# Kernel tuning notes

Measured on AMD Instinct MI355X. Metric: run time of the kernel, lower is better.

## Reference

```python
import jax, jax.numpy as jnp
import numpy as np

N, B, E, H, D, L, NT = 30000, 16, 60000, 128, 64, 2, 5


def _build_graph():
    rng = np.random.default_rng(0)
    ng = N // B
    row = rng.integers(0, N, size=E)
    g = row // ng
    col = g * ng + rng.integers(0, ng, size=E)  # bonds stay within a graph
    order = np.argsort(g, kind='stable')        # sort bonds by graph id
    row, col = row[order], col[order]
    edge_index = np.stack([row, col]).astype(np.int32)
    # bond graph: bonds adjacent iff they share an atom (vectorized _build_bond_graph)
    atoms = np.concatenate([row, col])
    bonds = np.concatenate([np.arange(E), np.arange(E)])
    o2 = np.argsort(atoms, kind='stable')
    sb = bonds[o2]
    counts = np.bincount(atoms, minlength=N)
    offs = np.concatenate([[0], np.cumsum(counts)[:-1]])
    sq = counts * counts
    total = int(sq.sum())
    gid = np.repeat(np.arange(N), sq)
    poff = np.concatenate([[0], np.cumsum(sq)[:-1]])
    pos = np.arange(total) - np.repeat(poff, sq)
    c, o = counts[gid], offs[gid]
    ii, jj = pos // c, pos % c
    mask = ii != jj
    bond_edge_index = np.stack([sb[o + ii][mask], sb[o + jj][mask]]).astype(np.int32)
    batch = np.repeat(np.arange(B), ng).astype(np.int32)
    return edge_index, bond_edge_index, batch


def setup_inputs() -> dict:
    edge_index, bond_edge_index, batch = _build_graph()
    key = jax.random.key(0)
    ks = jax.random.split(key, 16)
    s = 0.05
    n = lambda k, shp: jax.random.normal(k, shp, jnp.float32) * s
    return {
        'atom_features': jax.random.normal(ks[0], (N, H), jnp.float32),
        'atom_pos': jax.random.normal(ks[1], (N, 3), jnp.float32),
        'atomic_numbers': jax.random.randint(ks[2], (N,), 1, 20, jnp.int32),
        'batch': jnp.asarray(batch),
        'edge_index': jnp.asarray(edge_index),
        'bond_edge_index': jnp.asarray(bond_edge_index),
        'iw1': n(ks[3], (2 * H, D)), 'ib1': jnp.zeros((D,), jnp.float32),
        'iw2': n(ks[4], (D, D)), 'ib2': jnp.zeros((D,), jnp.float32),
        'emb': n(ks[5], (L, NT, D)),
        'mw1': n(ks[6], (L, 3 * D, D)), 'mb1': jnp.zeros((L, D), jnp.float32),
        'mw2': n(ks[7], (L, D, D)), 'mb2': jnp.zeros((L, D), jnp.float32),
        'uw1': n(ks[8], (L, 2 * D, D)), 'ub1': jnp.zeros((L, D), jnp.float32),
        'uw2': n(ks[9], (L, D, D)), 'ub2': jnp.zeros((L, D), jnp.float32),
        'num_graphs': B,
    }


def reference(atom_features, atom_pos, iw1, ib1, iw2, ib2, emb, mw1, mb1, mw2, mb2,
              uw1, ub1, uw2, ub2, atomic_numbers, batch, edge_index, bond_edge_index,
              num_graphs):
    row, col = edge_index
    hi, hj = atom_features[row], atom_features[col]  # [E, H] gathers
    # bond_init MLP
    x = jax.nn.silu(jnp.concatenate([hi, hj], -1) @ iw1 + ib1) @ iw2 + ib2  # [E, D]
    # _classify_bonds: cosine-similarity thresholds (order matters, matches torch)
    ni = jnp.maximum(jnp.linalg.norm(hi, axis=-1), 1e-8)
    nj = jnp.maximum(jnp.linalg.norm(hj, axis=-1), 1e-8)
    sim = jnp.sum(hi * hj, -1) / (ni * nj)
    bt = jnp.where(sim > 0.8, 1, 0)
    bt = jnp.where(sim > 0.9, 2, bt)
    bt = jnp.where(sim < 0.3, 3, bt)
    src, dst = bond_edge_index  # x_j = x[src], x_i = x[dst]; aggregate at dst
    nb = x.shape[0]
    deg = jax.ops.segment_sum(jnp.ones(src.shape, jnp.float32), dst, num_segments=nb)
    denom = jnp.maximum(deg, 1.0)[:, None]  # PyG mean aggr: 0 for isolated nodes
    for l in range(mw1.shape[0]):
        te = emb[l][bt]  # [E, D] bond-type embedding
        msg_in = jnp.concatenate([x[dst], x[src], te[dst]], -1)  # [BE, 3D]
        msg = jax.nn.silu(msg_in @ mw1[l] + mb1[l]) @ mw2[l] + mb2[l]
        aggr = jax.ops.segment_sum(msg, dst, num_segments=nb) / denom
        upd_in = jnp.concatenate([aggr, x], -1)
        x = x + jax.nn.silu(upd_in @ uw1[l] + ub1[l]) @ uw2[l] + ub2[l]
    # pooling: edges are sorted by graph, so repeat_interleave == batch[row]
    bond_batch = batch[row]
    cnt = jax.ops.segment_sum(jnp.ones((nb,), jnp.float32), bond_batch, num_segments=num_graphs)
    gfeat = jax.ops.segment_sum(x, bond_batch, num_segments=num_graphs) / jnp.maximum(cnt, 1.0)[:, None]
    return x, gfeat
```

## Files before the change

kernel.cpp:

```cpp
#include <hip/hip_runtime.h>
#include <cstdint>
#include <cstddef>

#define HDIM 128
#define DDIM 64
#define NTYPES 5
#define NGRAPHS 16
#define PCHUNK 128
#define EPB 64
#define APW 8

typedef __attribute__((ext_vector_type(8))) short short8;
typedef __attribute__((ext_vector_type(4))) float f32x4;

static __device__ __forceinline__ short8 as_s8(uint4 u) {
    return __builtin_bit_cast(short8, u);
}

static __device__ __forceinline__ float silu_f(float v) {
    return v * __builtin_amdgcn_rcpf(1.0f + __expf(-v));
}

static __device__ __forceinline__ float4 ld4(const float* p) {
    return *reinterpret_cast<const float4*>(p);
}

static __device__ __forceinline__ void st4(float* p, float4 v) {
    *reinterpret_cast<float4*>(p) = v;
}

static __device__ __forceinline__ float4 add4(float4 a, float4 b) {
    return make_float4(a.x + b.x, a.y + b.y, a.z + b.z, a.w + b.w);
}

static __device__ __forceinline__ void silu_acc4(float4& s, float4 v) {
    s.x += silu_f(v.x);
    s.y += silu_f(v.y);
    s.z += silu_f(v.z);
    s.w += silu_f(v.w);
}

static __device__ __forceinline__ unsigned int bf16r(float f) {
    unsigned int u = __float_as_uint(f);
    return (u + 0x7FFFu + ((u >> 16) & 1u)) >> 16;
}
static __device__ __forceinline__ unsigned int cvtpk(float a, float b) {
    unsigned int r;
    asm("v_cvt_pk_bf16_f32 %0, %1, %2" : "=v"(r) : "v"(a), "v"(b));
    return r;
}
static __device__ __forceinline__ uint4 pack8(const float* f) {
    uint4 r;
    r.x = cvtpk(f[0], f[1]);
    r.y = cvtpk(f[2], f[3]);
    r.z = cvtpk(f[4], f[5]);
    r.w = cvtpk(f[6], f[7]);
    return r;
}
static __device__ __forceinline__ void unpack8(uint4 u, float4& a, float4& b) {
    a.x = __uint_as_float(u.x << 16);
    a.y = __uint_as_float(u.x & 0xFFFF0000u);
    a.z = __uint_as_float(u.y << 16);
    a.w = __uint_as_float(u.y & 0xFFFF0000u);
    b.x = __uint_as_float(u.z << 16);
    b.y = __uint_as_float(u.z & 0xFFFF0000u);
    b.z = __uint_as_float(u.w << 16);
    b.w = __uint_as_float(u.w & 0xFFFF0000u);
}

static __device__ __forceinline__ void hilo8(const float* f, uint4& h, uint4& lo) {
    h = pack8(f);
    float4 a, b;
    unpack8(h, a, b);
    lo.x = cvtpk(f[0] - a.x, f[1] - a.y);
    lo.y = cvtpk(f[2] - a.z, f[3] - a.w);
    lo.z = cvtpk(f[4] - b.x, f[5] - b.y);
    lo.w = cvtpk(f[6] - b.z, f[7] - b.w);
}

static __device__ __forceinline__ int xcd_logical_block() {
    int chunk = (int)(gridDim.x >> 3);
    return (int)(blockIdx.x & 7) * chunk + (int)(blockIdx.x >> 3);
}

__global__ void __launch_bounds__(256) count_k(const int* __restrict__ bdst,
                                               int* __restrict__ cnt, int BE) {
    int i = blockIdx.x * 256 + threadIdx.x;
    if (i < BE)
        __hip_atomic_fetch_add(&cnt[bdst[i]], 1, __ATOMIC_RELAXED, __HIP_MEMORY_SCOPE_AGENT);
}

__global__ void __launch_bounds__(256) bsum_k(const int* __restrict__ cnt,
                                              int* __restrict__ bsum, int E) {
    __shared__ int red[256];
    int t = threadIdx.x;
    int i = blockIdx.x * 256 + t;
    red[t] = (i < E) ? cnt[i] : 0;
    __syncthreads();
    #pragma unroll
    for (int off = 128; off > 0; off >>= 1) {
        if (t < off) red[t] += red[t + off];
        __syncthreads();
    }
    if (t == 0) bsum[blockIdx.x] = red[0];
}

__global__ void __launch_bounds__(1024) bscan_k(const int* __restrict__ bsum,
                                                int* __restrict__ bpre, int NB) {
    __shared__ int sh[1024];
    int t = threadIdx.x;
    int v0 = (t < NB) ? bsum[t] : 0;
    sh[t] = v0;
    __syncthreads();
    for (int off = 1; off < 1024; off <<= 1) {
        int v = (t >= off) ? sh[t - off] : 0;
        __syncthreads();
        sh[t] += v;
        __syncthreads();
    }
    if (t < NB) bpre[t] = sh[t] - v0;
}

__global__ void __launch_bounds__(256) offs_k(const int* __restrict__ cnt,
                                              const int* __restrict__ bpre,
                                              int* __restrict__ offs,
                                              int* __restrict__ cursor, int E) {
    __shared__ int sh[256];
    int t = threadIdx.x;
    int i = blockIdx.x * 256 + t;
    int v0 = (i < E) ? cnt[i] : 0;
    sh[t] = v0;
    __syncthreads();
    for (int off = 1; off < 256; off <<= 1) {
        int v = (t >= off) ? sh[t - off] : 0;
        __syncthreads();
        sh[t] += v;
        __syncthreads();
    }
    int ex = sh[t] - v0 + bpre[blockIdx.x];
    if (i < E) { offs[i] = ex; cursor[i] = ex; }
    if (i == E - 1) offs[E] = ex + v0;
}

__global__ void __launch_bounds__(256) scatter_k(const int* __restrict__ bsrc,
                                                 const int* __restrict__ bdst,
                                                 int* __restrict__ cursor,
                                                 int* __restrict__ srclist, int BE) {
    int i = blockIdx.x * 256 + threadIdx.x;
    if (i < BE) {
        int d = bdst[i];
        int p = __hip_atomic_fetch_add(&cursor[d], 1, __ATOMIC_RELAXED,
                                       __HIP_MEMORY_SCOPE_AGENT);
        srclist[p] = bsrc[i];
    }
}

__global__ void __launch_bounds__(64) prep_k(const float* __restrict__ emb,
                                             const float* __restrict__ mw1,
                                             const float* __restrict__ mb1,
                                             const float* __restrict__ mw2,
                                             const float* __restrict__ mb2,
                                             const float* __restrict__ uw1,
                                             const float* __restrict__ uw2,
                                             const float* __restrict__ iw2,
                                             float* __restrict__ tt,
                                             float* __restrict__ b2u,
                                             uint4* __restrict__ fw2u,
                                             uint4* __restrict__ fu1b,
                                             uint4* __restrict__ fu2,
                                             uint4* __restrict__ fp,
                                             uint4* __restrict__ fiw2,
                                             uint4* __restrict__ fp0) {
    int b = blockIdx.x;
    int l = threadIdx.x;
    if (b < 10) {
        int ll = b / NTYPES, t = b % NTYPES;
        const float* embl = emb + (size_t)ll * NTYPES * DDIM + (size_t)t * DDIM;
        const float* w1 = mw1 + (size_t)ll * 192 * DDIM;
        float s = mb1[ll * DDIM + l];
        #pragma unroll 8
        for (int k = 0; k < DDIM; ++k)
            s = fmaf(embl[k], w1[(HDIM + k) * DDIM + l], s);
        tt[(size_t)b * DDIM + l] = s;
        return;
    }
    if (b < 12) {
        int ll = b - 10;
        const float* u1 = uw1 + (size_t)ll * 128 * DDIM;
        float s = 0.f;
        #pragma unroll 8
        for (int t = 0; t < DDIM; ++t)
            s = fmaf(mb2[ll * DDIM + t], u1[(size_t)t * DDIM + l], s);
        b2u[ll * DDIM + l] = s;
        return;
    }
    int pb = b - 12;
    int mat = pb >> 3, jt = (pb >> 1) & 3, ks = pb & 1;
    int k0 = ks * 32 + (l >> 4) * 8;
    int j = jt * 16 + (l & 15);
    float f[8];
    uint4* dst;
    if (mat <= 1) {
        const float* w2 = mw2 + (size_t)mat * DDIM * DDIM;
        const float* u1 = uw1 + (size_t)mat * 128 * DDIM;
        #pragma unroll
        for (int i = 0; i < 8; ++i) {
            float s = 0.f;
            #pragma unroll 8
            for (int t = 0; t < DDIM; ++t)
                s = fmaf(w2[(size_t)(k0 + i) * DDIM + t], u1[(size_t)t * DDIM + j], s);
            f[i] = s;
        }
        dst = fw2u + (size_t)mat * 1024;
    } else {
        const float* src;
        switch (mat) {
            case 2:  src = uw1 + 64 * 64;                   dst = fu1b;        break;
            case 3:  src = uw1 + 128 * 64 + 64 * 64;        dst = fu1b + 1024; break;
            case 4:  src = uw2;                             dst = fu2;         break;
            case 5:  src = uw2 + 4096;                      dst = fu2 + 1024;  break;
            case 6:  src = mw1 + (size_t)192 * 64;          dst = fp;          break;
            case 7:  src = mw1 + (size_t)192 * 64 + 64 * 64; dst = fp + 1024;  break;
            case 8:  src = iw2;                             dst = fiw2;        break;
            case 9:  src = mw1;                             dst = fp0;         break;
            default: src = mw1 + (size_t)64 * 64;           dst = fp0 + 1024;  break;
        }
        #pragma unroll
        for (int i = 0; i < 8; ++i) f[i] = src[(size_t)(k0 + i) * DDIM + j];
    }
    uint4 h, lo;
    hilo8(f, h, lo);
    size_t di = ((size_t)(jt * 2 + ks) * 64 + l) * 2;
    dst[di] = h;
    dst[di + 1] = lo;
}

static __device__ __forceinline__ int slotIdx(int row, int slot) {
    return row * 8 + (slot ^ (row & 7));
}

static __device__ __forceinline__ short8 ldFragA(const uint4* buf, int rowBase, int lane, int ks) {
    int row = rowBase + (lane & 15);
    int slot = ks * 4 + (lane >> 4);
    return as_s8(buf[slotIdx(row, slot)]);
}

static __device__ __forceinline__ void loadB(const uint4* __restrict__ frag, int jt, int lane,
                                             short8& h0, short8& h1, short8& l0, short8& l1) {
    const uint4* p0 = frag + ((size_t)(jt * 2 + 0) * 64 + lane) * 2;
    const uint4* p1 = frag + ((size_t)(jt * 2 + 1) * 64 + lane) * 2;
    h0 = as_s8(p0[0]); l0 = as_s8(p0[1]);
    h1 = as_s8(p1[0]); l1 = as_s8(p1[1]);
}

static __device__ __forceinline__ f32x4 gemm_tile(const uint4* Ahi, const uint4* Alo,
        int rowBase, int lane,
        short8 bh0, short8 bh1, short8 bl0, short8 bl1, f32x4 acc) {
    short8 ah0 = ldFragA(Ahi, rowBase, lane, 0);
    short8 ah1 = ldFragA(Ahi, rowBase, lane, 1);
    short8 al0 = ldFragA(Alo, rowBase, lane, 0);
    short8 al1 = ldFragA(Alo, rowBase, lane, 1);
    acc = __builtin_amdgcn_mfma_f32_16x16x32_bf16(ah0, bh0, acc, 0, 0, 0);
    acc = __builtin_amdgcn_mfma_f32_16x16x32_bf16(ah1, bh1, acc, 0, 0, 0);
    acc = __builtin_amdgcn_mfma_f32_16x16x32_bf16(al0, bh0, acc, 0, 0, 0);
    acc = __builtin_amdgcn_mfma_f32_16x16x32_bf16(al1, bh1, acc, 0, 0, 0);
    acc = __builtin_amdgcn_mfma_f32_16x16x32_bf16(ah0, bl0, acc, 0, 0, 0);
    acc = __builtin_amdgcn_mfma_f32_16x16x32_bf16(ah1, bl1, acc, 0, 0, 0);
    return acc;
}

__global__ void __launch_bounds__(256) atom_proj_k(
    const float* __restrict__ AF, const float* __restrict__ iw1,
    float* __restrict__ pa, float* __restrict__ qa, float* __restrict__ na, int N) {
    int lane = threadIdx.x & 63;
    int w = __builtin_amdgcn_readfirstlane((int)(threadIdx.x >> 6));
    int abase = blockIdx.x * (4 * APW) + w * APW;
    if (abase >= N) return;

    float accp[APW], accq[APW], nrm[APW];
    #pragma unroll
    for (int a = 0; a < APW; ++a) { accp[a] = 0.f; accq[a] = 0.f; nrm[a] = 0.f; }

    #pragma unroll 4
    for (int k = 0; k < HDIM; k += 4) {
        float wt[4], wb[4];
        #pragma unroll
        for (int kk = 0; kk < 4; ++kk) {
            wt[kk] = iw1[(size_t)(k + kk) * DDIM + lane];
            wb[kk] = iw1[(size_t)(HDIM + k + kk) * DDIM + lane];
        }
        #pragma unroll
        for (int a = 0; a < APW; ++a) {
            int aa = min(abase + a, N - 1);
            float4 hv = ld4(AF + (size_t)aa * HDIM + k);
            accp[a] = fmaf(hv.x, wt[0], accp[a]);
            accp[a] = fmaf(hv.y, wt[1], accp[a]);
            accp[a] = fmaf(hv.z, wt[2], accp[a]);
            accp[a] = fmaf(hv.w, wt[3], accp[a]);
            accq[a] = fmaf(hv.x, wb[0], accq[a]);
            accq[a] = fmaf(hv.y, wb[1], accq[a]);
            accq[a] = fmaf(hv.z, wb[2], accq[a]);
            accq[a] = fmaf(hv.w, wb[3], accq[a]);
            nrm[a] = fmaf(hv.x, hv.x, nrm[a]);
            nrm[a] = fmaf(hv.y, hv.y, nrm[a]);
            nrm[a] = fmaf(hv.z, hv.z, nrm[a]);
            nrm[a] = fmaf(hv.w, hv.w, nrm[a]);
        }
    }
    #pragma unroll
    for (int a = 0; a < APW; ++a) {
        int atom = abase + a;
        if (atom < N) {
            pa[(size_t)atom * DDIM + lane] = accp[a];
            qa[(size_t)atom * DDIM + lane] = accq[a];
            if (lane == 0) na[atom] = sqrtf(nrm[a]);
        }
    }
}

__global__ void __launch_bounds__(512, 4) bond_init2_k(
    const float* __restrict__ AF, const int* __restrict__ row, const int* __restrict__ col,
    const float* __restrict__ pa, const float* __restrict__ qa, const float* __restrict__ na,
    const float* __restrict__ b1, const uint4* __restrict__ fW2, const float* __restrict__ b2,
    const uint4* __restrict__ fP0,
    float* __restrict__ x, int* __restrict__ bt,
    float* __restrict__ pd, uint4* __restrict__ ps, int E) {
    __shared__ uint4 sAhi[512];
    __shared__ uint4 sAlo[512];
    __shared__ uint4 sXhi[512];
    __shared__ uint4 sXlo[512];
    int nEB = (E + EPB - 1) / EPB;
    int lb = xcd_logical_block();
    if (lb >= nEB) return;
    int tid = threadIdx.x;
    int lane = tid & 63;
    int w = __builtin_amdgcn_readfirstlane((int)(tid >> 6));
    int e0 = lb * EPB;

    {
        int dl = tid >> 3, q = tid & 7;
        int d = e0 + dl;
        bool ok = d < E;
        int dd = ok ? d : 0;
        int r = row[dd], c = col[dd];
        int jq = q * 8;

        const float* hi = AF + (size_t)r * HDIM + q * 16;
        const float* hj = AF + (size_t)c * HDIM + q * 16;
        float dt = 0.f;
        #pragma unroll
        for (int k = 0; k < 16; k += 4) {
            float4 a4 = ld4(hi + k), b4 = ld4(hj + k);
            dt += a4.x * b4.x + a4.y * b4.y + a4.z * b4.z + a4.w * b4.w;
        }
        dt += __shfl_xor(dt, 1, 64);
        dt += __shfl_xor(dt, 2, 64);
        dt += __shfl_xor(dt, 4, 64);
        if (q == 0 && ok) {
            float nr = fmaxf(na[r], 1e-8f), nc = fmaxf(na[c], 1e-8f);
            float sim = dt / (nr * nc);
            int t = 0;
            if (sim > 0.8f) t = 1;
            if (sim > 0.9f) t = 2;
            if (sim < 0.3f) t = 3;
            bt[d] = t;
        }

        const float* pr = pa + (size_t)r * DDIM + jq;
        const float* qc = qa + (size_t)c * DDIM + jq;
        float4 p0 = ld4(pr + 0), p1 = ld4(pr + 4);
        float4 q0 = ld4(qc + 0), q1 = ld4(qc + 4);
        float hv[8];
        hv[0] = silu_f(p0.x + q0.x + b1[jq + 0]);
        hv[1] = silu_f(p0.y + q0.y + b1[jq + 1]);
        hv[2] = silu_f(p0.z + q0.z + b1[jq + 2]);
        hv[3] = silu_f(p0.w + q0.w + b1[jq + 3]);
        hv[4] = silu_f(p1.x + q1.x + b1[jq + 4]);
        hv[5] = silu_f(p1.y + q1.y + b1[jq + 5]);
        hv[6] = silu_f(p1.z + q1.z + b1[jq + 6]);
        hv[7] = silu_f(p1.w + q1.w + b1[jq + 7]);
        if (!ok) {
            #pragma unroll
            for (int i = 0; i < 8; ++i) hv[i] = 0.f;
        }
        uint4 h4, l4;
        hilo8(hv, h4, l4);
        int si = slotIdx(dl, q);
        sAhi[si] = h4; sAlo[si] = l4;
    }
    int jt = w & 3, mh = w >> 2;
    short8 W2h0, W2h1, W2l0, W2l1;
    loadB(fW2, jt, lane, W2h0, W2h1, W2l0, W2l1);
    __syncthreads();

    int rb0 = mh * 32, rb1 = mh * 32 + 16;
    f32x4 z4 = {0.f, 0.f, 0.f, 0.f};
    f32x4 acc0 = gemm_tile(sAhi, sAlo, rb0, lane, W2h0, W2h1, W2l0, W2l1, z4);
    f32x4 acc1 = gemm_tile(sAhi, sAlo, rb1, lane, W2h0, W2h1, W2l0, W2l1, z4);
// ... 40 lines not shown
        int jd = jp * 16 + (lane & 15);
        #pragma unroll
        for (int mt = 0; mt < 4; ++mt) {
            f32x4 qq = (mt == 0) ? q0 : (mt == 1) ? q1 : (mt == 2) ? q2 : q3;
            #pragma unroll
            for (int r = 0; r < 4; ++r) {
                int rowi = mt * 16 + (lane >> 4) * 4 + r;
                int e = e0 + rowi;
                if (e < E) pd[(size_t)e * DDIM + jd] = qq[r];
            }
        }
    } else {
        int js = jp * 16 + (lane & 15);
        #pragma unroll
        for (int mt = 0; mt < 4; ++mt) {
            f32x4 qq = (mt == 0) ? q0 : (mt == 1) ? q1 : (mt == 2) ? q2 : q3;
            #pragma unroll
            for (int r = 0; r < 4; ++r) {
                int rowi = mt * 16 + (lane >> 4) * 4 + r;
                int ui = (rowi * 8 + ((js >> 3) ^ (rowi & 7))) * 8 + (js & 7);
                hA[ui] = (unsigned short)bf16r(qq[r]);
            }
        }
    }
    __syncthreads();
    {
        int dl = tid >> 3, q = tid & 7;
        int d = e0 + dl;
        if (d < E) ps[(size_t)d * 8 + q] = sAhi[slotIdx(dl, q)];
    }
}

__global__ void __launch_bounds__(256) proj_k(const float* __restrict__ x,
                                              const float* __restrict__ w1 ,
                                              float* __restrict__ pd, uint4* __restrict__ ps,
                                              int E) {
    int lane = threadIdx.x & 63;
    int w = __builtin_amdgcn_readfirstlane((int)(threadIdx.x >> 6));
    int e = blockIdx.x * EPB + lane;
    bool ok = e < E;
    int eidx = ok ? e : 0;
    int j0 = w * 16;
    const float* xr = x + (size_t)eidx * DDIM;

    float apd[16], aps[16];
    #pragma unroll
    for (int jj = 0; jj < 16; ++jj) { apd[jj] = 0.f; aps[jj] = 0.f; }
    #pragma unroll 2
    for (int c = 0; c < 16; ++c) {
        float4 v = ld4(xr + c * 4);
        float xv[4] = {v.x, v.y, v.z, v.w};
        #pragma unroll
        for (int kk = 0; kk < 4; ++kk) {
            int k = c * 4 + kk;
            const float* wd = w1 + (size_t)k * DDIM + j0;
            const float* wsv = w1 + (size_t)(DDIM + k) * DDIM + j0;
            #pragma unroll
            for (int jj = 0; jj < 16; ++jj) {
                apd[jj] = fmaf(xv[kk], wd[jj], apd[jj]);
                aps[jj] = fmaf(xv[kk], wsv[jj], aps[jj]);
            }
        }
    }
    if (ok) {
        float* pr = pd + (size_t)e * DDIM + j0;
        st4(pr + 0,  make_float4(apd[0],  apd[1],  apd[2],  apd[3]));
        st4(pr + 4,  make_float4(apd[4],  apd[5],  apd[6],  apd[7]));
        st4(pr + 8,  make_float4(apd[8],  apd[9],  apd[10], apd[11]));
        st4(pr + 12, make_float4(apd[12], apd[13], apd[14], apd[15]));
        ps[(size_t)e * 8 + 2 * w + 0] = pack8(aps + 0);
        ps[(size_t)e * 8 + 2 * w + 1] = pack8(aps + 8);
    }
}

__global__ void __launch_bounds__(512, 4) layer_k(
    float* __restrict__ x, const float* __restrict__ pd, const uint4* __restrict__ ps,
    const float* __restrict__ tt_l, const int* __restrict__ bt,
    const int* __restrict__ offs, const int* __restrict__ srclist,
    const int* __restrict__ cnt,
    const uint4* __restrict__ fW2u, const float* __restrict__ b2u,
    const uint4* __restrict__ fU1b, const float* __restrict__ ub1,
    const uint4* __restrict__ fU2, const float* __restrict__ ub2,
    const uint4* __restrict__ fP ,
    float* __restrict__ pdn, uint4* __restrict__ psn, int E) {
    __shared__ uint4 sAhi[512];
    __shared__ uint4 sAlo[512];
    __shared__ uint4 sXhi[512];
    __shared__ uint4 sXlo[512];
    __shared__ float degLDS[64];
    int nEB = (E + EPB - 1) / EPB;
    int lb = xcd_logical_block();
    if (lb >= nEB) return;
    int tid = threadIdx.x;
    int lane = tid & 63;
    int w = __builtin_amdgcn_readfirstlane((int)(tid >> 6));
    int e0 = lb * EPB;

    {
        int dl = tid >> 3, q = tid & 7;
        int d = e0 + dl;
        bool ok = d < E;
        int dd = ok ? d : 0;
        int jq = q * 8;
        const float* xr = x + (size_t)dd * DDIM + jq;
        float4 xv0 = ld4(xr + 0), xv1 = ld4(xr + 4);
        int dc = cnt[dd];
        const float* pr = pd + (size_t)dd * DDIM + jq;
        const float* tp = tt_l + (size_t)bt[dd] * DDIM + jq;
        float4 b0 = add4(ld4(pr + 0), ld4(tp + 0));
        float4 b1 = add4(ld4(pr + 4), ld4(tp + 4));
        float4 s0 = make_float4(0, 0, 0, 0), s1 = s0;
        int p0 = ok ? offs[d] : 0, p1 = ok ? offs[d + 1] : 0;
        int p = p0;
        for (; p + 4 <= p1; p += 4) {
            uint4 u0 = ps[(size_t)srclist[p + 0] * 8 + q];
            uint4 u1 = ps[(size_t)srclist[p + 1] * 8 + q];
            uint4 u2 = ps[(size_t)srclist[p + 2] * 8 + q];
            uint4 u3 = ps[(size_t)srclist[p + 3] * 8 + q];
            float4 a, b;
            unpack8(u0, a, b);
            silu_acc4(s0, add4(b0, a));
            silu_acc4(s1, add4(b1, b));
            unpack8(u1, a, b);
            silu_acc4(s0, add4(b0, a));
            silu_acc4(s1, add4(b1, b));
            unpack8(u2, a, b);
            silu_acc4(s0, add4(b0, a));
            silu_acc4(s1, add4(b1, b));
            unpack8(u3, a, b);
            silu_acc4(s0, add4(b0, a));
            silu_acc4(s1, add4(b1, b));
        }
        for (; p < p1; ++p) {
            uint4 u0 = ps[(size_t)srclist[p] * 8 + q];
            float4 a, b;
            unpack8(u0, a, b);
            silu_acc4(s0, add4(b0, a));
            silu_acc4(s1, add4(b1, b));
        }
        float inv = 1.0f / fmaxf((float)dc, 1.0f);
        float sv[8] = {s0.x * inv, s0.y * inv, s0.z * inv, s0.w * inv,
                       s1.x * inv, s1.y * inv, s1.z * inv, s1.w * inv};
        float xf[8] = {xv0.x, xv0.y, xv0.z, xv0.w, xv1.x, xv1.y, xv1.z, xv1.w};
        if (!ok) {
            #pragma unroll
            for (int i = 0; i < 8; ++i) { sv[i] = 0.f; xf[i] = 0.f; }
        }
        uint4 h4, l4;
        int si = slotIdx(dl, q);
        hilo8(sv, h4, l4);
        sAhi[si] = h4; sAlo[si] = l4;
        hilo8(xf, h4, l4);
        sXhi[si] = h4; sXlo[si] = l4;
        if (q == 0) degLDS[dl] = (ok && dc > 0) ? 1.0f : 0.0f;
    }
    int jt = w & 3, mh = w >> 2;
    short8 A2h0, A2h1, A2l0, A2l1;
    short8 U1h0, U1h1, U1l0, U1l1;
    loadB(fW2u, jt, lane, A2h0, A2h1, A2l0, A2l1);
    loadB(fU1b, jt, lane, U1h0, U1h1, U1l0, U1l1);
    __syncthreads();

    int rb0 = mh * 32, rb1 = mh * 32 + 16;
    f32x4 z4 = {0.f, 0.f, 0.f, 0.f};
    f32x4 acc0 = z4, acc1 = z4;
    acc0 = gemm_tile(sAhi, sAlo, rb0, lane, A2h0, A2h1, A2l0, A2l1, acc0);
    acc0 = gemm_tile(sXhi, sXlo, rb0, lane, U1h0, U1h1, U1l0, U1l1, acc0);
    acc1 = gemm_tile(sAhi, sAlo, rb1, lane, A2h0, A2h1, A2l0, A2l1, acc1);
    acc1 = gemm_tile(sXhi, sXlo, rb1, lane, U1h0, U1h1, U1l0, U1l1, acc1);
    __syncthreads();
    int j = jt * 16 + (lane & 15);
    float ub1j = ub1[j], b2uj = b2u[j];
    unsigned short* hA = (unsigned short*)sAhi;
    unsigned short* lA = (unsigned short*)sAlo;
    #pragma unroll
    for (int r = 0; r < 4; ++r) {
        int row = rb0 + (lane >> 4) * 4 + r;
        float hv = silu_f(acc0[r] + ub1j + degLDS[row] * b2uj);
        unsigned int hb = bf16r(hv);
        float lov = hv - __uint_as_float(hb << 16);
        int ui = (row * 8 + ((j >> 3) ^ (row & 7))) * 8 + (j & 7);
        hA[ui] = (unsigned short)hb;
        lA[ui] = (unsigned short)bf16r(lov);
    }
    #pragma unroll
    for (int r = 0; r < 4; ++r) {
        int row = rb1 + (lane >> 4) * 4 + r;
        float hv = silu_f(acc1[r] + ub1j + degLDS[row] * b2uj);
        unsigned int hb = bf16r(hv);
        float lov = hv - __uint_as_float(hb << 16);
        int ui = (row * 8 + ((j >> 3) ^ (row & 7))) * 8 + (j & 7);
        hA[ui] = (unsigned short)hb;
        lA[ui] = (unsigned short)bf16r(lov);
    }
    __syncthreads();

    short8 U2h0, U2h1, U2l0, U2l1;
    loadB(fU2, jt, lane, U2h0, U2h1, U2l0, U2l1);
    f32x4 o0 = gemm_tile(sAhi, sAlo, rb0, lane, U2h0, U2h1, U2l0, U2l1, z4);
    f32x4 o1 = gemm_tile(sAhi, sAlo, rb1, lane, U2h0, U2h1, U2l0, U2l1, z4);
    float ub2j = ub2[j];
    bool haveP = (fP != nullptr);
    unsigned short* hX = (unsigned short*)sXhi;
    unsigned short* lX = (unsigned short*)sXlo;
    #pragma unroll
    for (int r = 0; r < 4; ++r) {
        int row = rb0 + (lane >> 4) * 4 + r;
        int e = e0 + row;
        int ui = (row * 8 + ((j >> 3) ^ (row & 7))) * 8 + (j & 7);
        float xvv = __uint_as_float((unsigned int)hX[ui] << 16)
                  + __uint_as_float((unsigned int)lX[ui] << 16);
        float xn = xvv + o0[r] + ub2j;
        if (e < E) x[(size_t)e * DDIM + j] = xn;
        if (haveP) {
            unsigned int hb = bf16r(xn);
            float lov = xn - __uint_as_float(hb << 16);
            hX[ui] = (unsigned short)hb;
            lX[ui] = (unsigned short)bf16r(lov);
        }
    }
    #pragma unroll
    for (int r = 0; r < 4; ++r) {
        int row = rb1 + (lane >> 4) * 4 + r;
        int e = e0 + row;
        int ui = (row * 8 + ((j >> 3) ^ (row & 7))) * 8 + (j & 7);
        float xvv = __uint_as_float((unsigned int)hX[ui] << 16)
                  + __uint_as_float((unsigned int)lX[ui] << 16);
        float xn = xvv + o1[r] + ub2j;
        if (e < E) x[(size_t)e * DDIM + j] = xn;
        if (haveP) {
            unsigned int hb = bf16r(xn);
            float lov = xn - __uint_as_float(hb << 16);
            hX[ui] = (unsigned short)hb;
            lX[ui] = (unsigned short)bf16r(lov);
        }
    }
    if (!haveP) return;
    __syncthreads();

    const uint4* fPw = (w < 4) ? fP : (fP + 1024);
    int jp = w & 3;
    short8 Ph0, Ph1, Pl0, Pl1;
    loadB(fPw, jp, lane, Ph0, Ph1, Pl0, Pl1);
    f32x4 q0 = gemm_tile(sXhi, sXlo, 0,  lane, Ph0, Ph1, Pl0, Pl1, z4);
    f32x4 q1 = gemm_tile(sXhi, sXlo, 16, lane, Ph0, Ph1, Pl0, Pl1, z4);
    f32x4 q2 = gemm_tile(sXhi, sXlo, 32, lane, Ph0, Ph1, Pl0, Pl1, z4);
    f32x4 q3 = gemm_tile(sXhi, sXlo, 48, lane, Ph0, Ph1, Pl0, Pl1, z4);
    if (w < 4) {
        int jd = jp * 16 + (lane & 15);
        #pragma unroll
        for (int mt = 0; mt < 4; ++mt) {
            f32x4 qq = (mt == 0) ? q0 : (mt == 1) ? q1 : (mt == 2) ? q2 : q3;
            #pragma unroll
            for (int r = 0; r < 4; ++r) {
                int row = mt * 16 + (lane >> 4) * 4 + r;
                int e = e0 + row;
                if (e < E) pdn[(size_t)e * DDIM + jd] = qq[r];
            }
        }
    } else {
        int js = jp * 16 + (lane & 15);
        #pragma unroll
        for (int mt = 0; mt < 4; ++mt) {
            f32x4 qq = (mt == 0) ? q0 : (mt == 1) ? q1 : (mt == 2) ? q2 : q3;
            #pragma unroll
            for (int r = 0; r < 4; ++r) {
                int row = mt * 16 + (lane >> 4) * 4 + r;
                int ui = (row * 8 + ((js >> 3) ^ (row & 7))) * 8 + (js & 7);
                hA[ui] = (unsigned short)bf16r(qq[r]);
            }
        }
    }
    __syncthreads();
    {
        int dl = tid >> 3, q = tid & 7;
        int d = e0 + dl;
        if (d < E) psn[(size_t)d * 8 + q] = sAhi[slotIdx(dl, q)];
    }
}

__global__ void __launch_bounds__(256) pool_k(
    const float* __restrict__ x, const int* __restrict__ row,
    const int* __restrict__ batch, float* __restrict__ gfeat, int E) {
    int lane = threadIdx.x & 63;
    int esub = threadIdx.x >> 6;
    int e0 = blockIdx.x * PCHUNK;
    int e1 = min(e0 + PCHUNK, E);
    float sum = 0.f;
    int cur = -1;
    for (int e = e0 + esub; e < e1; e += 4) {
        int g = batch[row[e]];
        if (g != cur) {
            if (cur >= 0)
                __hip_atomic_fetch_add(&gfeat[cur * DDIM + lane], sum,
                                       __ATOMIC_RELAXED, __HIP_MEMORY_SCOPE_AGENT);
            cur = g;
            sum = 0.f;
        }
        sum += x[(size_t)e * DDIM + lane];
    }
    if (cur >= 0)
        __hip_atomic_fetch_add(&gfeat[cur * DDIM + lane], sum,
                               __ATOMIC_RELAXED, __HIP_MEMORY_SCOPE_AGENT);
}

static __device__ __forceinline__ int lower_bound_bb(const int* __restrict__ row,
                                                     const int* __restrict__ batch,
                                                     int E, int g) {
    int lo = 0, hi = E;
    while (lo < hi) {
        int m = (lo + hi) >> 1;
        if (batch[row[m]] < g) lo = m + 1; else hi = m;
    }
    return lo;
}

__global__ void __launch_bounds__(64) pool_final_k(
    const int* __restrict__ row, const int* __restrict__ batch,
    float* __restrict__ gfeat, int E) {
    int g = blockIdx.x, j = threadIdx.x;
    int s = lower_bound_bb(row, batch, E, g);
    int t = lower_bound_bb(row, batch, E, g + 1);
    float cnt = fmaxf((float)(t - s), 1.0f);
    gfeat[g * DDIM + j] /= cnt;
}

extern "C" void kernel_launch(void* const* d_in, const int* in_sizes, int n_in,
                              void* d_out, int out_size, void* d_ws, size_t ws_size,
                              hipStream_t stream) {
    (void)n_in; (void)out_size;
    const float* AF    = (const float*)d_in[0];
    const int*   batch = (const int*)d_in[3];
    const int*   edge_index      = (const int*)d_in[4];
    const int*   bond_edge_index = (const int*)d_in[5];
    const float* iw1 = (const float*)d_in[6];
    const float* ib1 = (const float*)d_in[7];
    const float* iw2 = (const float*)d_in[8];
    const float* ib2 = (const float*)d_in[9];
    const float* emb = (const float*)d_in[10];
    const float* mw1 = (const float*)d_in[11];
    const float* mb1 = (const float*)d_in[12];
    const float* mw2 = (const float*)d_in[13];
    const float* mb2 = (const float*)d_in[14];
    const float* uw1 = (const float*)d_in[15];
    const float* ub1 = (const float*)d_in[16];
    const float* uw2 = (const float*)d_in[17];
    const float* ub2 = (const float*)d_in[18];

    const int N  = in_sizes[0] / HDIM;
    const int E  = in_sizes[4] / 2;
    const int BE = in_sizes[5] / 2;
    const int NB = (E + 255) / 256;
    const int EB = (E + EPB - 1) / EPB;
    const int AB = (N + 4 * APW - 1) / (4 * APW);
    const int EBS = ((EB + 7) / 8) * 8;
    const int PB = (E + PCHUNK - 1) / PCHUNK;

    float* xout  = (float*)d_out;
    float* gfeat = xout + (size_t)E * DDIM;

    char* w = (char*)d_ws;
    float* tt       = (float*)w;  w += sizeof(float) * 2 * NTYPES * DDIM;
    float* b2u      = (float*)w;  w += sizeof(float) * 2 * DDIM;
    w = (char*)(((uintptr_t)w + 15) & ~(uintptr_t)15);
    uint4* fW2u     = (uint4*)w;  w += 2048 * sizeof(uint4);
    uint4* fU1b     = (uint4*)w;  w += 2048 * sizeof(uint4);
    uint4* fU2      = (uint4*)w;  w += 2048 * sizeof(uint4);
    uint4* fP       = (uint4*)w;  w += 2048 * sizeof(uint4);
    uint4* fIw2     = (uint4*)w;  w += 1024 * sizeof(uint4);
    uint4* fP0      = (uint4*)w;  w += 2048 * sizeof(uint4);
    int*   cnt      = (int*)w;    w += sizeof(int) * E;
    int*   offs     = (int*)w;    w += sizeof(int) * (E + 1);
    int*   cursor   = (int*)w;    w += sizeof(int) * E;
    int*   bt       = (int*)w;    w += sizeof(int) * E;
    int*   bsum     = (int*)w;    w += sizeof(int) * 1024;
    int*   bpre     = (int*)w;    w += sizeof(int) * 1024;
    int*   srclist  = (int*)w;    w += sizeof(int) * BE;
    w = (char*)(((uintptr_t)w + 15) & ~(uintptr_t)15);
    float* pd       = (float*)w;  w += sizeof(float) * (size_t)E * DDIM;
    uint4* ps       = (uint4*)w;  w += sizeof(unsigned short) * (size_t)E * DDIM;
    float* pa       = (float*)w;  w += sizeof(float) * (size_t)N * DDIM;
    float* qa       = (float*)w;  w += sizeof(float) * (size_t)N * DDIM;
    float* na       = (float*)w;  w += sizeof(float) * (size_t)N;
    w = (char*)(((uintptr_t)w + 15) & ~(uintptr_t)15);
    float* pd2      = (float*)w;  w += sizeof(float) * (size_t)E * DDIM;
    uint4* ps2      = (uint4*)w;  w += sizeof(unsigned short) * (size_t)E * DDIM;
    bool fuse_proj = ((size_t)(w - (char*)d_ws) <= ws_size);

    const int* row  = edge_index;
    const int* col  = edge_index + E;
    const int* bsrc = bond_edge_index;
    const int* bdst = bond_edge_index + BE;

    hipMemsetAsync(cnt, 0, (size_t)E * sizeof(int), stream);
    count_k<<<(BE + 255) / 256, 256, 0, stream>>>(bdst, cnt, BE);
    bsum_k<<<NB, 256, 0, stream>>>(cnt, bsum, E);
    bscan_k<<<1, 1024, 0, stream>>>(bsum, bpre, NB);
    offs_k<<<NB, 256, 0, stream>>>(cnt, bpre, offs, cursor, E);
    scatter_k<<<(BE + 255) / 256, 256, 0, stream>>>(bsrc, bdst, cursor, srclist, BE);

    prep_k<<<100, 64, 0, stream>>>(emb, mw1, mb1, mw2, mb2, uw1, uw2, iw2,
                                   tt, b2u, fW2u, fU1b, fU2, fP, fIw2, fP0);

    atom_proj_k<<<AB, 256, 0, stream>>>(AF, iw1, pa, qa, na, N);
    bond_init2_k<<<EBS, 512, 0, stream>>>(AF, row, col, pa, qa, na, ib1, fIw2, ib2,
                                          fP0, xout, bt, pd, ps, E);

    if (fuse_proj) {
        layer_k<<<EBS, 512, 0, stream>>>(
            xout, pd, ps, tt, bt, offs, srclist, cnt,
            fW2u, b2u, fU1b, ub1, fU2, ub2,
            fP, pd2, ps2, E);
        layer_k<<<EBS, 512, 0, stream>>>(
            xout, pd2, ps2, tt + NTYPES * DDIM, bt, offs, srclist, cnt,
            fW2u + 1024, b2u + DDIM, fU1b + 1024, ub1 + DDIM,
            fU2 + 1024, ub2 + DDIM,
            nullptr, nullptr, nullptr, E);
    } else {
        for (int l = 0; l < 2; ++l) {
            if (l > 0)
                proj_k<<<EB, 256, 0, stream>>>(xout, mw1 + (size_t)l * 192 * 64, pd, ps, E);
            layer_k<<<EBS, 512, 0, stream>>>(
                xout, pd, ps, tt + (size_t)l * NTYPES * DDIM, bt, offs, srclist, cnt,
                fW2u + (size_t)l * 1024, b2u + (size_t)l * DDIM,
                fU1b + (size_t)l * 1024, ub1 + (size_t)l * DDIM,
                fU2 + (size_t)l * 1024, ub2 + (size_t)l * DDIM,
                nullptr, nullptr, nullptr, E);
        }
    }

    hipMemsetAsync(gfeat, 0, NGRAPHS * DDIM * sizeof(float), stream);
    pool_k<<<PB, 256, 0, stream>>>(xout, row, batch, gfeat, E);
    pool_final_k<<<NGRAPHS, 64, 0, stream>>>(row, batch, gfeat, E);
}
```

Baseline: 315.2 us.

## Fuse pooling into last layer, MFMA atom projection, stage neighbor indices in LDS

Moves graph mean-pooling into the final layer_k epilogue, using LDS partial sums and atomics into gfeat, and drops the separate pool_k pass that re-read x. It rewrites atom_proj_k to use bf16 hi/lo split MFMA with iw1 fragments prepared in prep_k, in place of scalar FMA loops. It also stages each block's srclist slice in LDS before the neighbor gather, with a global-memory fallback when the slice exceeds capacity. The risks are extra LDS use and syncs in layer_k, possibly lowering occupancy, plus atomic contention and bf16-split precision in the projection.

```diff
diff --git a/kernel.cpp b/kernel.cpp
--- a/kernel.cpp
+++ b/kernel.cpp
@@ -6,9 +6,8 @@
 #define DDIM 64
 #define NTYPES 5
 #define NGRAPHS 16
-#define PCHUNK 128
 #define EPB 64
-#define APW 8
+#define SCAP 1024
 
 typedef __attribute__((ext_vector_type(8))) short short8;
 typedef __attribute__((ext_vector_type(4))) float f32x4;
@@ -163,6 +162,7 @@
                                              const float* __restrict__ uw1,
                                              const float* __restrict__ uw2,
                                              const float* __restrict__ iw2,
+                                             const float* __restrict__ iw1,
                                              float* __restrict__ tt,
                                              float* __restrict__ b2u,
                                              uint4* __restrict__ fw2u,
@@ -170,7 +170,8 @@
                                              uint4* __restrict__ fu2,
                                              uint4* __restrict__ fp,
                                              uint4* __restrict__ fiw2,
-                                             uint4* __restrict__ fp0) {
+                                             uint4* __restrict__ fp0,
+                                             uint4* __restrict__ fiw1) {
     int b = blockIdx.x;
     int l = threadIdx.x;
     if (b < 10) {
@@ -215,15 +216,19 @@
     } else {
         const float* src;
         switch (mat) {
-            case 2:  src = uw1 + 64 * 64;                   dst = fu1b;        break;
-            case 3:  src = uw1 + 128 * 64 + 64 * 64;        dst = fu1b + 1024; break;
-            case 4:  src = uw2;                             dst = fu2;         break;
-            case 5:  src = uw2 + 4096;                      dst = fu2 + 1024;  break;
-            case 6:  src = mw1 + (size_t)192 * 64;          dst = fp;          break;
-            case 7:  src = mw1 + (size_t)192 * 64 + 64 * 64; dst = fp + 1024;  break;
-            case 8:  src = iw2;                             dst = fiw2;        break;
-            case 9:  src = mw1;                             dst = fp0;         break;
-            default: src = mw1 + (size_t)64 * 64;           dst = fp0 + 1024;  break;
+            case 2:  src = uw1 + 64 * 64;                    dst = fu1b;        break;
+            case 3:  src = uw1 + 128 * 64 + 64 * 64;         dst = fu1b + 1024; break;
+            case 4:  src = uw2;                              dst = fu2;         break;
+            case 5:  src = uw2 + 4096;                       dst = fu2 + 1024;  break;
+            case 6:  src = mw1 + (size_t)192 * 64;           dst = fp;          break;
+            case 7:  src = mw1 + (size_t)192 * 64 + 64 * 64; dst = fp + 1024;   break;
+            case 8:  src = iw2;                              dst = fiw2;        break;
+            case 9:  src = mw1;                              dst = fp0;         break;
+            case 10: src = mw1 + (size_t)64 * 64;            dst = fp0 + 1024;  break;
+            case 11: src = iw1;                              dst = fiw1;        break;
+            case 12: src = iw1 + (size_t)64 * 64;            dst = fiw1 + 1024; break;
+            case 13: src = iw1 + (size_t)128 * 64;           dst = fiw1 + 2048; break;
+            default: src = iw1 + (size_t)192 * 64;           dst = fiw1 + 3072; break;
         }
         #pragma unroll
         for (int i = 0; i < 8; ++i) f[i] = src[(size_t)(k0 + i) * DDIM + j];
@@ -238,11 +243,19 @@
 static __device__ __forceinline__ int slotIdx(int row, int slot) {
     return row * 8 + (slot ^ (row & 7));
 }
+static __device__ __forceinline__ int slotIdx16(int row, int slot) {
+    return row * 16 + (slot ^ (row & 7));
+}
 
 static __device__ __forceinline__ short8 ldFragA(const uint4* buf, int rowBase, int lane, int ks) {
     int row = rowBase + (lane & 15);
     int slot = ks * 4 + (lane >> 4);
     return as_s8(buf[slotIdx(row, slot)]);
+}
+static __device__ __forceinline__ short8 ldFragA16(const uint4* buf, int rowBase, int lane, int slot0) {
+    int row = rowBase + (lane & 15);
+    int slot = slot0 + (lane >> 4);
+    return as_s8(buf[slotIdx16(row, slot)]);
 }
 
 static __device__ __forceinline__ void loadB(const uint4* __restrict__ frag, int jt, int lane,
@@ -269,51 +282,79 @@
     return acc;
 }
 
-__global__ void __launch_bounds__(256) atom_proj_k(
-    const float* __restrict__ AF, const float* __restrict__ iw1,
+static __device__ __forceinline__ f32x4 gemm_tile16(const uint4* Ahi, const uint4* Alo,
+        int rowBase, int lane, int sb,
+        short8 bh0, short8 bh1, short8 bl0, short8 bl1, f32x4 acc) {
+    short8 ah0 = ldFragA16(Ahi, rowBase, lane, sb + 0);
+    short8 ah1 = ldFragA16(Ahi, rowBase, lane, sb + 4);
+    short8 al0 = ldFragA16(Alo, rowBase, lane, sb + 0);
+    short8 al1 = ldFragA16(Alo, rowBase, lane, sb + 4);
+    acc = __builtin_amdgcn_mfma_f32_16x16x32_bf16(ah0, bh0, acc, 0, 0, 0);
+    acc = __builtin_amdgcn_mfma_f32_16x16x32_bf16(ah1, bh1, acc, 0, 0, 0);
+    acc = __builtin_amdgcn_mfma_f32_16x16x32_bf16(al0, bh0, acc, 0, 0, 0);
+    acc = __builtin_amdgcn_mfma_f32_16x16x32_bf16(al1, bh1, acc, 0, 0, 0);
+    acc = __builtin_amdgcn_mfma_f32_16x16x32_bf16(ah0, bl0, acc, 0, 0, 0);
+    acc = __builtin_amdgcn_mfma_f32_16x16x32_bf16(ah1, bl1, acc, 0, 0, 0);
+    return acc;
+}
+
+__global__ void __launch_bounds__(512) atom_proj_k(
+    const float* __restrict__ AF, const uint4* __restrict__ fIw1,
     float* __restrict__ pa, float* __restrict__ qa, float* __restrict__ na, int N) {
-    int lane = threadIdx.x & 63;
-    int w = __builtin_amdgcn_readfirstlane((int)(threadIdx.x >> 6));
-    int abase = blockIdx.x * (4 * APW) + w * APW;
-    if (abase >= N) return;
-
-    float accp[APW], accq[APW], nrm[APW];
+    __shared__ uint4 sHi[1024];
+    __shared__ uint4 sLo[1024];
+    int tid = threadIdx.x;
+    int lane = tid & 63;
+    int w = __builtin_amdgcn_readfirstlane((int)(tid >> 6));
+    int a0 = blockIdx.x * 64;
+
+    {
+        int dl = tid >> 3, q = tid & 7;
+        int a = a0 + dl;
+        bool ok = a < N;
+        const float* ar = AF + (size_t)(ok ? a : 0) * HDIM + q * 16;
+        float4 v0 = ld4(ar + 0), v1 = ld4(ar + 4), v2 = ld4(ar + 8), v3 = ld4(ar + 12);
+        float nrm = v0.x*v0.x + v0.y*v0.y + v0.z*v0.z + v0.w*v0.w
+                  + v1.x*v1.x + v1.y*v1.y + v1.z*v1.z + v1.w*v1.w
+                  + v2.x*v2.x + v2.y*v2.y + v2.z*v2.z + v2.w*v2.w
+                  + v3.x*v3.x + v3.y*v3.y + v3.z*v3.z + v3.w*v3.w;
+        nrm += __shfl_xor(nrm, 1, 64);
+        nrm += __shfl_xor(nrm, 2, 64);
+        nrm += __shfl_xor(nrm, 4, 64);
+        if (q == 0 && ok) na[a] = sqrtf(nrm);
+        float f0[8] = {v0.x, v0.y, v0.z, v0.w, v1.x, v1.y, v1.z, v1.w};
+        float f1[8] = {v2.x, v2.y, v2.z, v2.w, v3.x, v3.y, v3.z, v3.w};
+        if (!ok) {
+            #pragma unroll
+            for (int i = 0; i < 8; ++i) { f0[i] = 0.f; f1[i] = 0.f; }
+        }
+        uint4 h, l;
+        hilo8(f0, h, l);
+        int s0 = slotIdx16(dl, q * 2);
+        sHi[s0] = h; sLo[s0] = l;
+        hilo8(f1, h, l);
+        int s1 = slotIdx16(dl, q * 2 + 1);
+        sHi[s1] = h; sLo[s1] = l;
+    }
+    int jt = w & 3;
+    const uint4* m0 = fIw1 + ((w < 4) ? 0 : 2048);
+    short8 B0h0, B0h1, B0l0, B0l1, B1h0, B1h1, B1l0, B1l1;
+    loadB(m0, jt, lane, B0h0, B0h1, B0l0, B0l1);
+    loadB(m0 + 1024, jt, lane, B1h0, B1h1, B1l0, B1l1);
+    __syncthreads();
+
+    float* dst = (w < 4) ? pa : qa;
+    int j = jt * 16 + (lane & 15);
+    f32x4 z4 = {0.f, 0.f, 0.f, 0.f};
     #pragma unroll
-    for (int a = 0; a < APW; ++a) { accp[a] = 0.f; accq[a] = 0.f; nrm[a] = 0.f; }
-
-    #pragma unroll 4
-    for (int k = 0; k < HDIM; k += 4) {
-        float wt[4], wb[4];
+    for (int rt = 0; rt < 4; ++rt) {
+        f32x4 acc = gemm_tile16(sHi, sLo, rt * 16, lane, 0, B0h0, B0h1, B0l0, B0l1, z4);
+        acc = gemm_tile16(sHi, sLo, rt * 16, lane, 8, B1h0, B1h1, B1l0, B1l1, acc);
         #pragma unroll
-        for (int kk = 0; kk < 4; ++kk) {
-            wt[kk] = iw1[(size_t)(k + kk) * DDIM + lane];
-            wb[kk] = iw1[(size_t)(HDIM + k + kk) * DDIM + lane];
-        }
-        #pragma unroll
-        for (int a = 0; a < APW; ++a) {
-            int aa = min(abase + a, N - 1);
-            float4 hv = ld4(AF + (size_t)aa * HDIM + k);
-            accp[a] = fmaf(hv.x, wt[0], accp[a]);
-            accp[a] = fmaf(hv.y, wt[1], accp[a]);
-            accp[a] = fmaf(hv.z, wt[2], accp[a]);
-            accp[a] = fmaf(hv.w, wt[3], accp[a]);
-            accq[a] = fmaf(hv.x, wb[0], accq[a]);
-            accq[a] = fmaf(hv.y, wb[1], accq[a]);
-            accq[a] = fmaf(hv.z, wb[2], accq[a]);
-            accq[a] = fmaf(hv.w, wb[3], accq[a]);
-            nrm[a] = fmaf(hv.x, hv.x, nrm[a]);
-            nrm[a] = fmaf(hv.y, hv.y, nrm[a]);
-            nrm[a] = fmaf(hv.z, hv.z, nrm[a]);
-            nrm[a] = fmaf(hv.w, hv.w, nrm[a]);
-        }
-    }
-    #pragma unroll
-    for (int a = 0; a < APW; ++a) {
-        int atom = abase + a;
-        if (atom < N) {
-            pa[(size_t)atom * DDIM + lane] = accp[a];
-            qa[(size_t)atom * DDIM + lane] = accq[a];
-            if (lane == 0) na[atom] = sqrtf(nrm[a]);
+        for (int r = 0; r < 4; ++r) {
+            int rowi = rt * 16 + (lane >> 4) * 4 + r;
+            int a = a0 + rowi;
+            if (a < N) dst[(size_t)a * DDIM + j] = acc[r];
         }
     }
 }
@@ -520,12 +561,16 @@
     const uint4* __restrict__ fU1b, const float* __restrict__ ub1,
     const uint4* __restrict__ fU2, const float* __restrict__ ub2,
     const uint4* __restrict__ fP ,
-    float* __restrict__ pdn, uint4* __restrict__ psn, int E) {
+    float* __restrict__ pdn, uint4* __restrict__ psn, int E,
+    const int* __restrict__ erow, const int* __restrict__ gbatch,
+    float* __restrict__ gfeat, int doPool) {
     __shared__ uint4 sAhi[512];
     __shared__ uint4 sAlo[512];
     __shared__ uint4 sXhi[512];
     __shared__ uint4 sXlo[512];
     __shared__ float degLDS[64];
+    __shared__ int   gidLDS[64];
+    __shared__ int   sIdx[SCAP];
     int nEB = (E + EPB - 1) / EPB;
     int lb = xcd_logical_block();
     if (lb >= nEB) return;
@@ -533,6 +578,7 @@
     int lane = tid & 63;
     int w = __builtin_amdgcn_readfirstlane((int)(tid >> 6));
     int e0 = lb * EPB;
+    int pb0 = offs[e0];
 
     {
         int dl = tid >> 3, q = tid & 7;
@@ -543,38 +589,75 @@
         const float* xr = x + (size_t)dd * DDIM + jq;
         float4 xv0 = ld4(xr + 0), xv1 = ld4(xr + 4);
         int dc = cnt[dd];
+        int rAtom = (doPool && ok) ? erow[dd] : 0;
         const float* pr = pd + (size_t)dd * DDIM + jq;
         const float* tp = tt_l + (size_t)bt[dd] * DDIM + jq;
         float4 b0 = add4(ld4(pr + 0), ld4(tp + 0));
         float4 b1 = add4(ld4(pr + 4), ld4(tp + 4));
+        int p0v = ok ? offs[d] : pb0, p1v = ok ? offs[d + 1] : pb0;
+
+        int emax = min(e0 + EPB, E);
+        int pT = offs[emax] - pb0;
+        for (int i = tid; i < pT && i < SCAP; i += 512) sIdx[i] = srclist[pb0 + i];
+        __syncthreads();
+
         float4 s0 = make_float4(0, 0, 0, 0), s1 = s0;
-        int p0 = ok ? offs[d] : 0, p1 = ok ? offs[d + 1] : 0;
-        int p = p0;
-        for (; p + 4 <= p1; p += 4) {
-            uint4 u0 = ps[(size_t)srclist[p + 0] * 8 + q];
-            uint4 u1 = ps[(size_t)srclist[p + 1] * 8 + q];
-            uint4 u2 = ps[(size_t)srclist[p + 2] * 8 + q];
-            uint4 u3 = ps[(size_t)srclist[p + 3] * 8 + q];
-            float4 a, b;
-            unpack8(u0, a, b);
-            silu_acc4(s0, add4(b0, a));
-            silu_acc4(s1, add4(b1, b));
-            unpack8(u1, a, b);
-            silu_acc4(s0, add4(b0, a));
-            silu_acc4(s1, add4(b1, b));
-            unpack8(u2, a, b);
-            silu_acc4(s0, add4(b0, a));
-            silu_acc4(s1, add4(b1, b));
-            unpack8(u3, a, b);
-            silu_acc4(s0, add4(b0, a));
-            silu_acc4(s1, add4(b1, b));
-        }
-        for (; p < p1; ++p) {
-            uint4 u0 = ps[(size_t)srclist[p] * 8 + q];
-            float4 a, b;
-            unpack8(u0, a, b);
-            silu_acc4(s0, add4(b0, a));
-            silu_acc4(s1, add4(b1, b));
+        if (p1v - pb0 <= SCAP) {
+            int li = p0v - pb0, le = p1v - pb0;
+            for (; li + 4 <= le; li += 4) {
+                uint4 u0 = ps[(size_t)sIdx[li + 0] * 8 + q];
+                uint4 u1 = ps[(size_t)sIdx[li + 1] * 8 + q];
+                uint4 u2 = ps[(size_t)sIdx[li + 2] * 8 + q];
+                uint4 u3 = ps[(size_t)sIdx[li + 3] * 8 + q];
+                float4 a, b;
+                unpack8(u0, a, b);
+                silu_acc4(s0, add4(b0, a));
+                silu_acc4(s1, add4(b1, b));
+                unpack8(u1, a, b);
+                silu_acc4(s0, add4(b0, a));
+                silu_acc4(s1, add4(b1, b));
+                unpack8(u2, a, b);
+                silu_acc4(s0, add4(b0, a));
+                silu_acc4(s1, add4(b1, b));
+                unpack8(u3, a, b);
+                silu_acc4(s0, add4(b0, a));
+                silu_acc4(s1, add4(b1, b));
+            }
+            for (; li < le; ++li) {
+                uint4 u0 = ps[(size_t)sIdx[li] * 8 + q];
+                float4 a, b;
+                unpack8(u0, a, b);
+                silu_acc4(s0, add4(b0, a));
+                silu_acc4(s1, add4(b1, b));
+            }
+        } else {
+            int p = p0v;
+            for (; p + 4 <= p1v; p += 4) {
+                uint4 u0 = ps[(size_t)srclist[p + 0] * 8 + q];
+                uint4 u1 = ps[(size_t)srclist[p + 1] * 8 + q];
+                uint4 u2 = ps[(size_t)srclist[p + 2] * 8 + q];
+                uint4 u3 = ps[(size_t)srclist[p + 3] * 8 + q];
+                float4 a, b;
+                unpack8(u0, a, b);
+                silu_acc4(s0, add4(b0, a));
+                silu_acc4(s1, add4(b1, b));
+                unpack8(u1, a, b);
+                silu_acc4(s0, add4(b0, a));
+                silu_acc4(s1, add4(b1, b));
+                unpack8(u2, a, b);
+                silu_acc4(s0, add4(b0, a));
+                silu_acc4(s1, add4(b1, b));
+                unpack8(u3, a, b);
+                silu_acc4(s0, add4(b0, a));
+                silu_acc4(s1, add4(b1, b));
+            }
+            for (; p < p1v; ++p) {
+                uint4 u0 = ps[(size_t)srclist[p] * 8 + q];
+                float4 a, b;
+                unpack8(u0, a, b);
+                silu_acc4(s0, add4(b0, a));
+                silu_acc4(s1, add4(b1, b));
+            }
         }
         float inv = 1.0f / fmaxf((float)dc, 1.0f);
         float sv[8] = {s0.x * inv, s0.y * inv, s0.z * inv, s0.w * inv,
@@ -590,7 +673,10 @@
         sAhi[si] = h4; sAlo[si] = l4;
         hilo8(xf, h4, l4);
         sXhi[si] = h4; sXlo[si] = l4;
-        if (q == 0) degLDS[dl] = (ok && dc > 0) ? 1.0f : 0.0f;
+        if (q == 0) {
+            degLDS[dl] = (ok && dc > 0) ? 1.0f : 0.0f;
+            gidLDS[dl] = (doPool && ok) ? gbatch[rAtom] : -1;
+        }
     }
     int jt = w & 3, mh = w >> 2;
     short8 A2h0, A2h1, A2l0, A2l1;
@@ -641,6 +727,7 @@
     bool haveP = (fP != nullptr);
     unsigned short* hX = (unsigned short*)sXhi;
     unsigned short* lX = (unsigned short*)sXlo;
+    float xnv0[4], xnv1[4];
     #pragma unroll
     for (int r = 0; r < 4; ++r) {
         int row = rb0 + (lane >> 4) * 4 + r;
@@ -649,6 +736,7 @@
         float xvv = __uint_as_float((unsigned int)hX[ui] << 16)
                   + __uint_as_float((unsigned int)lX[ui] << 16);
         float xn = xvv + o0[r] + ub2j;
+        xnv0[r] = xn;
         if (e < E) x[(size_t)e * DDIM + j] = xn;
         if (haveP) {
             unsigned int hb = bf16r(xn);
@@ -665,6 +753,7 @@
         float xvv = __uint_as_float((unsigned int)hX[ui] << 16)
                   + __uint_as_float((unsigned int)lX[ui] << 16);
         float xn = xvv + o1[r] + ub2j;
+        xnv1[r] = xn;
         if (e < E) x[(size_t)e * DDIM + j] = xn;
         if (haveP) {
             unsigned int hb = bf16r(xn);
@@ -673,7 +762,51 @@
             lX[ui] = (unsigned short)bf16r(lov);
         }
     }
-    if (!haveP) return;
+    if (!haveP) {
+        if (doPool) {
+            __syncthreads();
+            float* poolB = (float*)sAhi;
+            if (tid < 256) poolB[tid] = 0.f;
+            __syncthreads();
+            int gid0 = gidLDS[0];
+            bool uni = (gidLDS[EPB - 1] == gid0);
+            if (uni) {
+                float s = xnv0[0] + xnv0[1] + xnv0[2] + xnv0[3]
+                        + xnv1[0] + xnv1[1] + xnv1[2] + xnv1[3];
+                atomicAdd(&poolB[j], s);
+            } else {
+                #pragma unroll
+                for (int r = 0; r < 4; ++r) {
+                    int row = rb0 + (lane >> 4) * 4 + r;
+                    int g = gidLDS[row];
+                    if (g >= 0) {
+                        int sl = g - gid0;
+                        if (sl < 4) atomicAdd(&poolB[sl * DDIM + j], xnv0[r]);
+                        else atomicAdd(&gfeat[(size_t)g * DDIM + j], xnv0[r]);
+                    }
+                }
+                #pragma unroll
+                for (int r = 0; r < 4; ++r) {
+                    int row = rb1 + (lane >> 4) * 4 + r;
+                    int g = gidLDS[row];
+                    if (g >= 0) {
+                        int sl = g - gid0;
+                        if (sl < 4) atomicAdd(&poolB[sl * DDIM + j], xnv1[r]);
+                        else atomicAdd(&gfeat[(size_t)g * DDIM + j], xnv1[r]);
+                    }
+                }
+            }
+            __syncthreads();
+            if (tid < 256) {
+                int sl = tid >> 6;
+                int g = gid0 + sl;
+                float v = poolB[tid];
+                if (v != 0.f && g < NGRAPHS)
+                    atomicAdd(&gfeat[(size_t)g * DDIM + (tid & 63)], v);
+            }
+        }
+        return;
+    }
     __syncthreads();
 
     const uint4* fPw = (w < 4) ? fP : (fP + 1024);
@@ -715,31 +848,6 @@
         int d = e0 + dl;
         if (d < E) psn[(size_t)d * 8 + q] = sAhi[slotIdx(dl, q)];
     }
-}
-
-__global__ void __launch_bounds__(256) pool_k(
-    const float* __restrict__ x, const int* __restrict__ row,
-    const int* __restrict__ batch, float* __restrict__ gfeat, int E) {
-    int lane = threadIdx.x & 63;
-    int esub = threadIdx.x >> 6;
-    int e0 = blockIdx.x * PCHUNK;
-    int e1 = min(e0 + PCHUNK, E);
-    float sum = 0.f;
-    int cur = -1;
-    for (int e = e0 + esub; e < e1; e += 4) {
-        int g = batch[row[e]];
-        if (g != cur) {
-            if (cur >= 0)
-                __hip_atomic_fetch_add(&gfeat[cur * DDIM + lane], sum,
-                                       __ATOMIC_RELAXED, __HIP_MEMORY_SCOPE_AGENT);
-            cur = g;
-            sum = 0.f;
-        }
-        sum += x[(size_t)e * DDIM + lane];
-    }
-    if (cur >= 0)
-        __hip_atomic_fetch_add(&gfeat[cur * DDIM + lane], sum,
-                               __ATOMIC_RELAXED, __HIP_MEMORY_SCOPE_AGENT);
 }
 
 static __device__ __forceinline__ int lower_bound_bb(const int* __restrict__ row,
@@ -790,9 +898,8 @@
     const int BE = in_sizes[5] / 2;
     const int NB = (E + 255) / 256;
     const int EB = (E + EPB - 1) / EPB;
-    const int AB = (N + 4 * APW - 1) / (4 * APW);
+    const int APB = (N + 63) / 64;
     const int EBS = ((EB + 7) / 8) * 8;
-    const int PB = (E + PCHUNK - 1) / PCHUNK;
 
     float* xout  = (float*)d_out;
     float* gfeat = xout + (size_t)E * DDIM;
@@ -807,6 +914,7 @@
     uint4* fP       = (uint4*)w;  w += 2048 * sizeof(uint4);
     uint4* fIw2     = (uint4*)w;  w += 1024 * sizeof(uint4);
     uint4* fP0      = (uint4*)w;  w += 2048 * sizeof(uint4);
+    uint4* fIw1     = (uint4*)w;  w += 4096 * sizeof(uint4);
     int*   cnt      = (int*)w;    w += sizeof(int) * E;
     int*   offs     = (int*)w;    w += sizeof(int) * (E + 1);
     int*   cursor   = (int*)w;    w += sizeof(int) * E;
@@ -837,23 +945,25 @@
     offs_k<<<NB, 256, 0, stream>>>(cnt, bpre, offs, cursor, E);
     scatter_k<<<(BE + 255) / 256, 256, 0, stream>>>(bsrc, bdst, cursor, srclist, BE);
 
-    prep_k<<<100, 64, 0, stream>>>(emb, mw1, mb1, mw2, mb2, uw1, uw2, iw2,
-                                   tt, b2u, fW2u, fU1b, fU2, fP, fIw2, fP0);
-
-    atom_proj_k<<<AB, 256, 0, stream>>>(AF, iw1, pa, qa, na, N);
+    prep_k<<<132, 64, 0, stream>>>(emb, mw1, mb1, mw2, mb2, uw1, uw2, iw2, iw1,
+                                   tt, b2u, fW2u, fU1b, fU2, fP, fIw2, fP0, fIw1);
+
+    atom_proj_k<<<APB, 512, 0, stream>>>(AF, fIw1, pa, qa, na, N);
     bond_init2_k<<<EBS, 512, 0, stream>>>(AF, row, col, pa, qa, na, ib1, fIw2, ib2,
                                           fP0, xout, bt, pd, ps, E);
+
+    hipMemsetAsync(gfeat, 0, NGRAPHS * DDIM * sizeof(float), stream);
 
     if (fuse_proj) {
         layer_k<<<EBS, 512, 0, stream>>>(
             xout, pd, ps, tt, bt, offs, srclist, cnt,
             fW2u, b2u, fU1b, ub1, fU2, ub2,
-            fP, pd2, ps2, E);
+            fP, pd2, ps2, E, row, batch, gfeat, 0);
         layer_k<<<EBS, 512, 0, stream>>>(
             xout, pd2, ps2, tt + NTYPES * DDIM, bt, offs, srclist, cnt,
             fW2u + 1024, b2u + DDIM, fU1b + 1024, ub1 + DDIM,
             fU2 + 1024, ub2 + DDIM,
-            nullptr, nullptr, nullptr, E);
+            nullptr, nullptr, nullptr, E, row, batch, gfeat, 1);
     } else {
         for (int l = 0; l < 2; ++l) {
             if (l > 0)
@@ -863,11 +973,9 @@
                 fW2u + (size_t)l * 1024, b2u + (size_t)l * DDIM,
                 fU1b + (size_t)l * 1024, ub1 + (size_t)l * DDIM,
                 fU2 + (size_t)l * 1024, ub2 + (size_t)l * DDIM,
-                nullptr, nullptr, nullptr, E);
-        }
-    }
-
-    hipMemsetAsync(gfeat, 0, NGRAPHS * DDIM * sizeof(float), stream);
-    pool_k<<<PB, 256, 0, stream>>>(xout, row, batch, gfeat, E);
+                nullptr, nullptr, nullptr, E, row, batch, gfeat, l == 1 ? 1 : 0);
+        }
+    }
+
     pool_final_k<<<NGRAPHS, 64, 0, stream>>>(row, batch, gfeat, E);
 }
```

Result: faster. 285.3 us (-9.5%).
